# Performance work log

Measured on AMD Instinct MI355X. Metric: run time of the kernel, lower is better.

## Reference

```python
import jax, jax.numpy as jnp
import numpy as np

B, W = 131072, 32
N_SCEN, SDIM = 19, 16
EMBED_DIM, COMP_DIM = 768, 64
INPUT_DIM = EMBED_DIM + N_SCEN * SDIM  # 1072


def setup_inputs() -> dict:
    key = jax.random.key(0)
    k1, k2, k3, k4, k5, k6 = jax.random.split(key, 6)
    intent_embedding = jax.random.normal(k1, (B, EMBED_DIM), dtype=jnp.float32)
    scenario_ids = jax.random.randint(k2, (B, W), 0, N_SCEN, dtype=jnp.int32)
    # Prefix mask: the torch loop iterates the first int(mask.sum()) slots,
    # so the mask must be a contiguous run of ones.
    lengths = jax.random.randint(k3, (B,), 1, W + 1)
    scenario_mask = (jnp.arange(W)[None, :] < lengths[:, None]).astype(jnp.float32)
    # Parameters (init: normal std=0.01, zero biases)
    scenario_table = 0.01 * jax.random.normal(k4, (N_SCEN, SDIM), dtype=jnp.float32)
    W1 = 0.01 * jax.random.normal(k5, (INPUT_DIM, COMP_DIM), dtype=jnp.float32)
    b1 = jnp.zeros((COMP_DIM,), dtype=jnp.float32)
    W2 = 0.01 * jax.random.normal(k6, (COMP_DIM, 1), dtype=jnp.float32)
    b2 = jnp.zeros((1,), dtype=jnp.float32)
    return {
        "intent_embedding": intent_embedding,
        "scenario_ids": scenario_ids,
        "scenario_mask": scenario_mask,
        "scenario_table": scenario_table,
        "W1": W1, "b1": b1, "W2": W2, "b2": b2,
    }


def reference(intent_embedding, scenario_ids, scenario_mask, scenario_table, W1, b1, W2, b2):
    # Embedding lookup: [B, W, SDIM]
    embeds = scenario_table[scenario_ids]
    masked = embeds * scenario_mask[:, :, None]
    # Vectorized scatter-add into per-scenario bins: [B, N_SCEN, SDIM]
    batch_idx = jnp.arange(scenario_ids.shape[0])[:, None]
    bag3 = jnp.zeros(
        (scenario_ids.shape[0], N_SCEN, SDIM), dtype=embeds.dtype
    ).at[batch_idx, scenario_ids].add(masked)
    counts = scenario_mask.sum(axis=1, keepdims=True)
    bag_vec = bag3.reshape(scenario_ids.shape[0], N_SCEN * SDIM) / jnp.maximum(counts, 1.0)
    combined = jnp.concatenate([intent_embedding, bag_vec], axis=1)  # [B, 1072]
    h = jax.nn.relu(combined @ W1 + b1)  # dropout is identity in eval mode
    return jnp.tanh(h @ W2 + b2)  # [B, 1]
```

## Files before the change

kernel.cpp:

```cpp
#include <hip/hip_runtime.h>
#include <hip/hip_bf16.h>
#include <math.h>

using short8 = __attribute__((ext_vector_type(8))) short;
using f32x4  = __attribute__((ext_vector_type(4))) float;
using fv4    = __attribute__((ext_vector_type(4))) float;

#define EMB 768
#define CD  64
#define NSCEN 19
#define KSTEPS 24
#define NCHUNKS (25 * 4)
#define QB 14336

__device__ __forceinline__ ushort f2bf(float x) {
    unsigned u = __float_as_uint(x);
    u += 0x7FFFu + ((u >> 16) & 1u);
    return (ushort)(u >> 16);
}

__device__ __forceinline__ uint cvt2(float x, float y) {
    __hip_bfloat162 h = __float22bfloat162_rn(make_float2(x, y));
    union { __hip_bfloat162 h; uint u; } c;
    c.h = h;
    return c.u;
}

__global__ void prep_W1T(const float* __restrict__ table,
                         const float* __restrict__ W1,
                         ushort* __restrict__ W1T) {
    int e = blockIdx.x * 256 + threadIdx.x;
    if (e >= NCHUNKS * 512) return;
    int chunk = e >> 9, r = e & 511;
    int lane = r >> 3, j = r & 7;
    int ks = chunk >> 2, ct = chunk & 3;
    int col = ct * 16 + (lane & 15);
    int k = ks * 32 + ((lane >> 4) << 3) + j;
    float v = 0.f;
    if (k < EMB) {
        v = W1[(size_t)k * CD + col];
    } else {
        int s = k - EMB;
        if (s < NSCEN) {
            for (int d = 0; d < 16; ++d)
                v += table[s * 16 + d] * W1[(size_t)(EMB + s * 16 + d) * CD + col];
        }
    }
    W1T[e] = f2bf(v);
}

__global__ __launch_bounds__(512, 4)
void scorer_mfma(const float* __restrict__ emb,
                 const int* __restrict__ ids,
                 const float* __restrict__ mask,
                 const ushort* __restrict__ W1T,
                 const float* __restrict__ b1,
                 const float* __restrict__ W2,
                 const float* __restrict__ b2,
                 float* __restrict__ out) {
    __shared__ __align__(16) ushort Bq[2][QB];
    __shared__ __align__(16) ushort bagb[256][32];
    float* bagf = (float*)&Bq[1][0];

    const int t    = threadIdx.x;
    const int w    = t >> 6;
    const int lane = t & 63;
    const int lr   = lane & 15;
    const int lg   = lane >> 4;
    const int row0 = blockIdx.x * 256;

    uint4 f0, f1, f2, f3;
#define ISSUE_FILL(qs) do {                                                  \
    const uint* _g = (const uint*)((const char*)W1T + (size_t)(qs) * 4096);  \
    f0 = *(const uint4*)(_g + (t)        * 4);                               \
    f1 = *(const uint4*)(_g + (t + 512)  * 4);                               \
    f2 = *(const uint4*)(_g + (t + 1024) * 4);                               \
    if (t < 256) f3 = *(const uint4*)(_g + (t + 1536) * 4);                  \
} while (0)
#define WRITE_FILL(bufi) do {                                                \
    uint* _l = (uint*)&Bq[bufi][0];                                          \
    *(uint4*)(_l + (t)        * 4) = f0;                                     \
    *(uint4*)(_l + (t + 512)  * 4) = f1;                                     \
    *(uint4*)(_l + (t + 1024) * 4) = f2;                                     \
    if (t < 256) *(uint4*)(_l + (t + 1536) * 4) = f3;                        \
} while (0)

    ISSUE_FILL(0);

    if (t < 256) {
#pragma unroll
        for (int s = 0; s < NSCEN; ++s) bagf[t * 21 + s] = 0.f;
        const int*   idrow = ids  + (size_t)(row0 + t) * 32;
        const float* mrow  = mask + (size_t)(row0 + t) * 32;
        float cnt = 0.f;
#pragma unroll 2
        for (int q = 0; q < 8; ++q) {
            int4   i4 = ((const int4*)idrow)[q];
            float4 m4 = ((const float4*)mrow)[q];
            bagf[t * 21 + i4.x] += m4.x; cnt += m4.x;
            bagf[t * 21 + i4.y] += m4.y; cnt += m4.y;
            bagf[t * 21 + i4.z] += m4.z; cnt += m4.z;
            bagf[t * 21 + i4.w] += m4.w; cnt += m4.w;
        }
        float rc = 1.0f / fmaxf(cnt, 1.0f);
#pragma unroll
        for (int s = 0; s < 32; ++s)
            bagb[t][s] = (s < NSCEN) ? f2bf(bagf[t * 21 + s] * rc) : (ushort)0;
    }

    WRITE_FILL(0);
    ISSUE_FILL(6);
    __syncthreads();

    const float* ap = emb + (size_t)(row0 + w * 32 + lr) * EMB + (lg << 3);

    f32x4 acc[2][4];
#pragma unroll
    for (int i = 0; i < 2; ++i)
#pragma unroll
        for (int j = 0; j < 4; ++j) acc[i][j] = (f32x4)0.f;

    fv4    aA[2][2], aB[2][2];
    short8 bqr[4];

#define LOADA(dst, kks) do {                                   \
    const float* _p = ap + (kks) * 32;                         \
    dst[0][0] = *(const fv4*)(_p);                             \
    dst[0][1] = *(const fv4*)(_p + 4);                         \
    dst[1][0] = *(const fv4*)(_p + 16 * EMB);                  \
    dst[1][1] = *(const fv4*)(_p + 16 * EMB + 4);              \
} while (0)

#define LDSB(bufi, ksl) do {                                   \
    const ushort* _l = &Bq[bufi][(ksl) * 2048 + lane * 8];     \
    bqr[0] = *(const short8*)(_l);                             \
    bqr[1] = *(const short8*)(_l + 512);                       \
    bqr[2] = *(const short8*)(_l + 1024);                      \
    bqr[3] = *(const short8*)(_l + 1536);                      \
} while (0)

#define STEP(areg) do {                                                     \
    short8 _fa[2];                                                          \
    _Pragma("unroll")                                                       \
    for (int _rt = 0; _rt < 2; ++_rt) {                                     \
        union { uint u[4]; short8 s; } _c;                                  \
        _c.u[0] = cvt2(areg[_rt][0][0], areg[_rt][0][1]);                   \
        _c.u[1] = cvt2(areg[_rt][0][2], areg[_rt][0][3]);                   \
        _c.u[2] = cvt2(areg[_rt][1][0], areg[_rt][1][1]);                   \
        _c.u[3] = cvt2(areg[_rt][1][2], areg[_rt][1][3]);                   \
        _fa[_rt] = _c.s;                                                    \
    }                                                                       \
    _Pragma("unroll")                                                       \
    for (int _rt = 0; _rt < 2; ++_rt) {                                     \
        acc[_rt][0] = __builtin_amdgcn_mfma_f32_16x16x32_bf16(_fa[_rt], bqr[0], acc[_rt][0], 0, 0, 0); \
        acc[_rt][1] = __builtin_amdgcn_mfma_f32_16x16x32_bf16(_fa[_rt], bqr[1], acc[_rt][1], 0, 0, 0); \
        acc[_rt][2] = __builtin_amdgcn_mfma_f32_16x16x32_bf16(_fa[_rt], bqr[2], acc[_rt][2], 0, 0, 0); \
        acc[_rt][3] = __builtin_amdgcn_mfma_f32_16x16x32_bf16(_fa[_rt], bqr[3], acc[_rt][3], 0, 0, 0); \
    }                                                                       \
} while (0)

#define QUARTER(bufi, qs) do {                                              \
    _Pragma("unroll")                                                       \
    for (int _ksl = 0; _ksl < 6; ++_ksl) {                                  \
        const int _ks = (qs) + _ksl;                                        \
        LDSB(bufi, _ksl);                                                   \
        if ((_ks & 1) == 0) {                                               \
            if (_ks + 1 <= 23) LOADA(aB, _ks + 1);                          \
            STEP(aA);                                                       \
        } else {                                                            \
            if (_ks + 1 <= 23) LOADA(aA, _ks + 1);                          \
            STEP(aB);                                                       \
        }                                                                   \
    }                                                                       \
} while (0)

    LOADA(aA, 0);

    WRITE_FILL(1);
    ISSUE_FILL(12);
    QUARTER(0, 0);
    __syncthreads();

    WRITE_FILL(0);
    ISSUE_FILL(18);
    QUARTER(1, 6);
    __syncthreads();

    WRITE_FILL(1);
    QUARTER(0, 12);
    __syncthreads();

    QUARTER(1, 18);
    {
        short8 ab[2];
        ab[0] = *(const short8*)&bagb[w * 32 + lr][lg << 3];
        ab[1] = *(const short8*)&bagb[w * 32 + 16 + lr][lg << 3];
        LDSB(1, 6);
#pragma unroll
        for (int rt = 0; rt < 2; ++rt) {
            acc[rt][0] = __builtin_amdgcn_mfma_f32_16x16x32_bf16(ab[rt], bqr[0], acc[rt][0], 0, 0, 0);
            acc[rt][1] = __builtin_amdgcn_mfma_f32_16x16x32_bf16(ab[rt], bqr[1], acc[rt][1], 0, 0, 0);
            acc[rt][2] = __builtin_amdgcn_mfma_f32_16x16x32_bf16(ab[rt], bqr[2], acc[rt][2], 0, 0, 0);
            acc[rt][3] = __builtin_amdgcn_mfma_f32_16x16x32_bf16(ab[rt], bqr[3], acc[rt][3], 0, 0, 0);
        }
    }

    float b1v[4], w2v[4];
#pragma unroll
    for (int ct = 0; ct < 4; ++ct) {
        int c = ct * 16 + lr;
        b1v[ct] = b1[c];
        w2v[ct] = W2[c];
    }
    const float b2v = b2[0];
#pragma unroll
    for (int rt = 0; rt < 2; ++rt) {
#pragma unroll
        for (int r = 0; r < 4; ++r) {
            float p = 0.f;
#pragma unroll
            for (int ct = 0; ct < 4; ++ct) {
                float h = acc[rt][ct][r] + b1v[ct];
                p += fmaxf(h, 0.f) * w2v[ct];
            }
            p += __shfl_xor(p, 1);
            p += __shfl_xor(p, 2);
            p += __shfl_xor(p, 4);
            p += __shfl_xor(p, 8);
            if (lr == 0)
                out[row0 + w * 32 + rt * 16 + (lg << 2) + r] = tanhf(p + b2v);
        }
    }
#undef ISSUE_FILL
#undef WRITE_FILL
#undef LOADA
#undef LDSB
#undef STEP
#undef QUARTER
}

extern "C" void kernel_launch(void* const* d_in, const int* in_sizes, int n_in,
                              void* d_out, int out_size, void* d_ws, size_t ws_size,
                              hipStream_t stream) {
    const float* emb   = (const float*)d_in[0];
    const int*   ids   = (const int*)d_in[1];
    const float* mask  = (const float*)d_in[2];
    const float* table = (const float*)d_in[3];
    const float* W1    = (const float*)d_in[4];
    const float* b1    = (const float*)d_in[5];
    const float* W2    = (const float*)d_in[6];
    const float* b2    = (const float*)d_in[7];
    float* out  = (float*)d_out;
    ushort* W1T = (ushort*)d_ws;

    prep_W1T<<<200, 256, 0, stream>>>(table, W1, W1T);
    const int nblocks = out_size / 256;
    scorer_mfma<<<nblocks, 512, 0, stream>>>(emb, ids, mask, W1T, b1, W2, b2, out);
}
```

Before: 95.39 us.

## Compute scenario histogram in registers across all waves and hoist loads

Replaces the LDS-based scatter histogram, which ran on half the threads, with a per-lane register histogram using compare-select. Every wave handles its own 32 rows, each split across two lanes and combined with a cross-lane shuffle. The first A-tile and id/mask loads are also moved to the top of the kernel so their latency overlaps the weight fill. This removes serialized LDS read-modify-write traffic but adds many compare/add ALU ops and more register pressure.

```diff
diff --git a/kernel.cpp b/kernel.cpp
--- a/kernel.cpp
+++ b/kernel.cpp
@@ -59,8 +59,7 @@
                  const float* __restrict__ b2,
                  float* __restrict__ out) {
     __shared__ __align__(16) ushort Bq[2][QB];
-    __shared__ __align__(16) ushort bagb[256][32];
-    float* bagf = (float*)&Bq[1][0];
+    __shared__ __align__(16) ushort bagb[8][32][32];
 
     const int t    = threadIdx.x;
     const int w    = t >> 6;
@@ -68,6 +67,25 @@
     const int lr   = lane & 15;
     const int lg   = lane >> 4;
     const int row0 = blockIdx.x * 256;
+
+    const int hrow = row0 + w * 32 + (lane & 31);
+    const int*   idrow = ids  + (size_t)hrow * 32 + (lane >> 5) * 16;
+    const float* mrow  = mask + (size_t)hrow * 32 + (lane >> 5) * 16;
+    int4   iv0 = ((const int4*)idrow)[0],  iv1 = ((const int4*)idrow)[1],
+           iv2 = ((const int4*)idrow)[2],  iv3 = ((const int4*)idrow)[3];
+    float4 mv0 = ((const float4*)mrow)[0], mv1 = ((const float4*)mrow)[1],
+           mv2 = ((const float4*)mrow)[2], mv3 = ((const float4*)mrow)[3];
+
+    const float* ap = emb + (size_t)(row0 + w * 32 + lr) * EMB + (lg << 3);
+    fv4 aA[2][2], aB[2][2];
+#define LOADA(dst, kks) do {                                   \
+    const float* _p = ap + (kks) * 32;                         \
+    dst[0][0] = *(const fv4*)(_p);                             \
+    dst[0][1] = *(const fv4*)(_p + 4);                         \
+    dst[1][0] = *(const fv4*)(_p + 16 * EMB);                  \
+    dst[1][1] = *(const fv4*)(_p + 16 * EMB + 4);              \
+} while (0)
+    LOADA(aA, 0);
 
     uint4 f0, f1, f2, f3;
 #define ISSUE_FILL(qs) do {                                                  \
@@ -84,53 +102,53 @@
     *(uint4*)(_l + (t + 1024) * 4) = f2;                                     \
     if (t < 256) *(uint4*)(_l + (t + 1536) * 4) = f3;                        \
 } while (0)
-
     ISSUE_FILL(0);
 
-    if (t < 256) {
-#pragma unroll
-        for (int s = 0; s < NSCEN; ++s) bagf[t * 21 + s] = 0.f;
-        const int*   idrow = ids  + (size_t)(row0 + t) * 32;
-        const float* mrow  = mask + (size_t)(row0 + t) * 32;
-        float cnt = 0.f;
-#pragma unroll 2
-        for (int q = 0; q < 8; ++q) {
-            int4   i4 = ((const int4*)idrow)[q];
-            float4 m4 = ((const float4*)mrow)[q];
-            bagf[t * 21 + i4.x] += m4.x; cnt += m4.x;
-            bagf[t * 21 + i4.y] += m4.y; cnt += m4.y;
-            bagf[t * 21 + i4.z] += m4.z; cnt += m4.z;
-            bagf[t * 21 + i4.w] += m4.w; cnt += m4.w;
-        }
+    float bin[NSCEN];
+#pragma unroll
+    for (int s = 0; s < NSCEN; ++s) bin[s] = 0.f;
+    float cnt = 0.f;
+#define HSLOT(idv, mvv) do {                                   \
+    cnt += mvv;                                                \
+    _Pragma("unroll")                                          \
+    for (int s = 0; s < NSCEN; ++s)                            \
+        bin[s] += (idv == s) ? mvv : 0.f;                      \
+} while (0)
+    HSLOT(iv0.x, mv0.x); HSLOT(iv0.y, mv0.y); HSLOT(iv0.z, mv0.z); HSLOT(iv0.w, mv0.w);
+    HSLOT(iv1.x, mv1.x); HSLOT(iv1.y, mv1.y); HSLOT(iv1.z, mv1.z); HSLOT(iv1.w, mv1.w);
+    HSLOT(iv2.x, mv2.x); HSLOT(iv2.y, mv2.y); HSLOT(iv2.z, mv2.z); HSLOT(iv2.w, mv2.w);
+    HSLOT(iv3.x, mv3.x); HSLOT(iv3.y, mv3.y); HSLOT(iv3.z, mv3.z); HSLOT(iv3.w, mv3.w);
+#undef HSLOT
+    cnt += __shfl_xor(cnt, 32);
+#pragma unroll
+    for (int s = 0; s < NSCEN; ++s) bin[s] += __shfl_xor(bin[s], 32);
+    {
         float rc = 1.0f / fmaxf(cnt, 1.0f);
-#pragma unroll
-        for (int s = 0; s < 32; ++s)
-            bagb[t][s] = (s < NSCEN) ? f2bf(bagf[t * 21 + s] * rc) : (ushort)0;
+        if (lane < 32) {
+            uint u[16];
+#pragma unroll
+            for (int p = 0; p < 9; ++p) u[p] = cvt2(bin[2 * p] * rc, bin[2 * p + 1] * rc);
+            u[9] = cvt2(bin[18] * rc, 0.f);
+#pragma unroll
+            for (int p = 10; p < 16; ++p) u[p] = 0u;
+            ushort* bp = &bagb[w][lane][0];
+#pragma unroll
+            for (int q = 0; q < 4; ++q)
+                *(uint4*)(bp + q * 8) = make_uint4(u[4 * q], u[4 * q + 1], u[4 * q + 2], u[4 * q + 3]);
+        }
     }
 
     WRITE_FILL(0);
     ISSUE_FILL(6);
     __syncthreads();
 
-    const float* ap = emb + (size_t)(row0 + w * 32 + lr) * EMB + (lg << 3);
-
     f32x4 acc[2][4];
 #pragma unroll
     for (int i = 0; i < 2; ++i)
 #pragma unroll
         for (int j = 0; j < 4; ++j) acc[i][j] = (f32x4)0.f;
 
-    fv4    aA[2][2], aB[2][2];
     short8 bqr[4];
-
-#define LOADA(dst, kks) do {                                   \
-    const float* _p = ap + (kks) * 32;                         \
-    dst[0][0] = *(const fv4*)(_p);                             \
-    dst[0][1] = *(const fv4*)(_p + 4);                         \
-    dst[1][0] = *(const fv4*)(_p + 16 * EMB);                  \
-    dst[1][1] = *(const fv4*)(_p + 16 * EMB + 4);              \
-} while (0)
-
 #define LDSB(bufi, ksl) do {                                   \
     const ushort* _l = &Bq[bufi][(ksl) * 2048 + lane * 8];     \
     bqr[0] = *(const short8*)(_l);                             \
@@ -174,8 +192,6 @@
     }                                                                       \
 } while (0)
 
-    LOADA(aA, 0);
-
     WRITE_FILL(1);
     ISSUE_FILL(12);
     QUARTER(0, 0);
@@ -193,8 +209,8 @@
     QUARTER(1, 18);
     {
         short8 ab[2];
-        ab[0] = *(const short8*)&bagb[w * 32 + lr][lg << 3];
-        ab[1] = *(const short8*)&bagb[w * 32 + 16 + lr][lg << 3];
+        ab[0] = *(const short8*)&bagb[w][lr][lg << 3];
+        ab[1] = *(const short8*)&bagb[w][16 + lr][lg << 3];
         LDSB(1, 6);
 #pragma unroll
         for (int rt = 0; rt < 2; ++rt) {
```

Result: faster. 91.48 us (-4.1%).
